# Performance work log

Measured on AMD Instinct MI355X. Metric: run time of the kernel, lower is better.

## Reference

```python
import jax, jax.numpy as jnp
import numpy as np
import math

B, S, D, H = 1, 2048, 2048, 16
DH, DHID, DKER = 128, 256, 128  # dim_head, dim_hid, dim_ker


def _uniform(k, shape, a):
    return jax.random.uniform(k, shape, jnp.float32, -a, a)


def setup_inputs() -> dict:
    key = jax.random.key(0)
    ks = jax.random.split(key, 14)
    a1 = math.sqrt(6.0 / (DH + DHID))
    a2 = math.sqrt(6.0 / (DKER + DHID))
    a3 = math.sqrt(6.0 / (2 * DKER))
    return {
        "x_t": jax.random.normal(ks[0], (B, S, D), jnp.float32),
        "q": jax.random.normal(ks[1], (B, S, D), jnp.float32),
        "k": jax.random.normal(ks[2], (B, S, D), jnp.float32),
        "v": jax.random.normal(ks[3], (B, S, D), jnp.float32),
        "lr_attn_mask": jax.random.bernoulli(ks[4], 0.5, (B, H, S, S)),
        "sparse_norms_lse": jax.random.normal(ks[5], (B, H, S, 1), jnp.float32),
        "sparse_attn_weights": jax.random.normal(ks[6], (B, H, S, S), jnp.float32),
        "lambda_constant": 0,
        "kernel_q_mat1": _uniform(ks[7], (H, DH, DHID), a1),
        "kernel_k_mat1": _uniform(ks[8], (H, DH, DHID), a1),
        "kernel_q_mat2": _uniform(ks[9], (H, DHID, DKER), a2),
        "kernel_k_mat2": _uniform(ks[10], (H, DHID, DKER), a2),
        "interaction_k": _uniform(ks[11], (H, DKER, DKER), a3),
        "scalingD": jnp.full((1, H, 1, DKER), 1e-4, jnp.float32),
        "scalingD2": jnp.full((1, H, 1, DKER), 1e-4, jnp.float32),
    }


def _gelu(x):
    return jax.nn.gelu(x, approximate=False)  # matches torch F.gelu default


def reference(x_t, q, k, v, lr_attn_mask, sparse_norms_lse, sparse_attn_weights,
              lambda_constant, kernel_q_mat1, kernel_k_mat1, kernel_q_mat2,
              kernel_k_mat2, interaction_k, scalingD, scalingD2):
    Bq, Sq, Dq = q.shape
    dh = Dq // H
    # [B,S,D] -> [B,H,S,dh]
    qh = q.reshape(Bq, Sq, H, dh).transpose(0, 2, 1, 3)
    kh = k.reshape(Bq, Sq, H, dh).transpose(0, 2, 1, 3)
    vh = v.reshape(Bq, Sq, H, dh).transpose(0, 2, 1, 3)

    # per-head two-layer feature maps (dropout is identity at eval)
    qf = _gelu(jnp.einsum('bhsd,hde->bhse', qh, kernel_q_mat1))
    qf = _gelu(jnp.einsum('bhse,hef->bhsf', qf, kernel_q_mat2))
    kf = _gelu(jnp.einsum('bhsd,hde->bhse', kh, kernel_k_mat1))
    kf = jnp.abs(scalingD) * _gelu(jnp.einsum('bhse,hef->bhsf', kf, kernel_k_mat2))
    kf = kf + jnp.einsum('bhse,hef->bhsf', kf, interaction_k) * scalingD2

    # masked non-negative kernel scores [B,H,S,S]
    scores = jnp.einsum('bhse,bhte->bhst', jnp.abs(qf), jnp.abs(kf))
    m = lr_attn_mask.astype(scores.dtype)
    scores = m * scores

    lr_norms_lse = jnp.log(scores.sum(axis=-1, keepdims=True) + 1e-6)
    norm_factor_lse = jnp.logaddexp(lr_norms_lse, sparse_norms_lse)

    logits = jnp.log(scores + 1e-6) * m + (1.0 - m) * sparse_attn_weights
    attn = jnp.exp(logits - norm_factor_lse)

    out = jnp.einsum('bhst,bhtd->bhsd', attn, vh)
    return out.transpose(0, 2, 1, 3).reshape(Bq, Sq, Dq)
```

## Files before the change

### kernel.cpp

```cpp
#include <hip/hip_runtime.h>
#include <hip/hip_bf16.h>
#include <math.h>

#define H_    16
#define S_    2048
#define D_    2048
#define DH_   128
#define DHID_ 256
#define DKER_ 128

typedef __attribute__((ext_vector_type(8))) short short8v;
typedef __attribute__((ext_vector_type(4))) float float4v;
typedef __attribute__((ext_vector_type(4))) int int4v;

static __device__ __forceinline__ short f2bf(float x){
  union { float f; unsigned u; } v; v.f = x;
  unsigned r = v.u + 0x7fffu + ((v.u >> 16) & 1u);
  return (short)(r >> 16);
}
static __device__ __forceinline__ float gelu_f(float x){
  return 0.5f * x * (1.0f + erff(x * 0.70710678118654752440f));
}
static __device__ __forceinline__ float4v mfma16(short8v a, short8v b, float4v c){
  return __builtin_amdgcn_mfma_f32_16x16x32_bf16(a, b, c, 0, 0, 0);
}
static __device__ __forceinline__ unsigned cvtpk(float lo, float hi){
  unsigned d;
  asm("v_cvt_pk_bf16_f32 %0, %1, %2" : "=v"(d) : "v"(lo), "v"(hi));
  return d;
}
static __device__ __forceinline__ void glds16(const void* g, void* l){
  __builtin_amdgcn_global_load_lds(
      (const __attribute__((address_space(1))) void*)g,
      (__attribute__((address_space(3))) void*)l, 16, 0, 0);
}

__global__ void detect_mask_kernel(const unsigned int* mw, int* flag){
  int t = threadIdx.x;
  int bin = 1, f32ok = 1, odd0 = 1;
  for (int i = t; i < 1024; i += 256){
    unsigned w = mw[i];
    if (w > 1u) bin = 0;
    if (w != 0u && w != 0x3F800000u) f32ok = 0;
    if ((i & 1) && w != 0u) odd0 = 0;
  }
  __shared__ int sb, sf, so;
  if (t == 0){ sb = 1; sf = 1; so = 1; }
  __syncthreads();
  if (!bin)  atomicAnd(&sb, 0);
  if (!f32ok) atomicAnd(&sf, 0);
  if (!odd0) atomicAnd(&so, 0);
  __syncthreads();
  if (t == 0) *flag = sb ? (so ? 3 : 0) : (sf ? 2 : 1);
}

__global__ __launch_bounds__(256) void prep_kernel(
    const void* __restrict__ mask, const int* __restrict__ flagp,
    unsigned* __restrict__ MP,
    const float* __restrict__ w1q, short* __restrict__ W1qT,
    const float* __restrict__ w1k, short* __restrict__ W1kT,
    const float* __restrict__ w2q, short* __restrict__ W2qT,
    const float* __restrict__ w2k, short* __restrict__ W2kT,
    const float* __restrict__ ik,  short* __restrict__ IKT,
    const float* __restrict__ v,   short* __restrict__ V3){
  __shared__ float tile[32][33];
  int b = blockIdx.x;
  int tid = threadIdx.x;

  if (b < 8192){
    int flag = *flagp;
    size_t w = (size_t)b * 256 + tid;
    size_t base = w * 32;
    unsigned bits = 0;
    if (flag == 0){
      const int4v* m = (const int4v*)((const int*)mask + base);
      #pragma unroll
      for (int c = 0; c < 8; ++c){
        int4v x = m[c];
        bits |= (x[0] != 0 ? 1u : 0u) << (c*4+0);
        bits |= (x[1] != 0 ? 1u : 0u) << (c*4+1);
        bits |= (x[2] != 0 ? 1u : 0u) << (c*4+2);
        bits |= (x[3] != 0 ? 1u : 0u) << (c*4+3);
      }
    } else if (flag == 1){
      const int4v* m = (const int4v*)((const unsigned char*)mask + base);
      #pragma unroll
      for (int c = 0; c < 2; ++c){
        int4v x = m[c];
        #pragma unroll
        for (int e = 0; e < 4; ++e){
          unsigned u = (unsigned)x[e];
          #pragma unroll
          for (int bb = 0; bb < 4; ++bb)
            bits |= (((u >> (8*bb)) & 0xffu) != 0 ? 1u : 0u) << (c*16 + e*4 + bb);
        }
      }
    } else if (flag == 2){
      const float4v* m = (const float4v*)((const float*)mask + base);
      #pragma unroll
      for (int c = 0; c < 8; ++c){
        float4v x = m[c];
        bits |= (x[0] != 0.0f ? 1u : 0u) << (c*4+0);
        bits |= (x[1] != 0.0f ? 1u : 0u) << (c*4+1);
        bits |= (x[2] != 0.0f ? 1u : 0u) << (c*4+2);
        bits |= (x[3] != 0.0f ? 1u : 0u) << (c*4+3);
      }
    } else {
      const int4v* m = (const int4v*)((const int*)mask + 2*base);
      #pragma unroll
      for (int c = 0; c < 16; ++c){
        int4v x = m[c];
        bits |= (x[0] != 0 ? 1u : 0u) << (c*2+0);
        bits |= (x[2] != 0 ? 1u : 0u) << (c*2+1);
      }
    }
    MP[w] = bits;
    return;
  }
  b -= 8192;
  if (b < 512){
    int h = b >> 5, bx = b & 31;
    int d = tid & 127;
    int t32 = bx * 2 + (tid >> 7);
    const float* src = v + (size_t)(t32 * 32) * D_ + h * DH_ + d;
    short* dst = V3 + (((size_t)h * (S_/32) + t32) * 128 + d) * 32;
    #pragma unroll
    for (int o = 0; o < 4; ++o){
      short8v w;
      #pragma unroll
      for (int j = 0; j < 8; ++j){
        int trel = (j < 4) ? (o * 4 + j) : (16 + o * 4 + (j - 4));
        w[j] = f2bf(src[(size_t)trel * D_]);
      }
      *(short8v*)(dst + o * 8) = w;
    }
    return;
  }
  b -= 512;
  const float* src; short* dst; int R, C, bx, by, h;
  if (b < 512){        src = w1q; dst = W1qT; R = DH_;  C = DHID_;
                       bx = b & 7; by = (b >> 3) & 3; h = b >> 5; }
  else if (b < 1024){  b -= 512;  src = w1k; dst = W1kT; R = DH_;  C = DHID_;
                       bx = b & 7; by = (b >> 3) & 3; h = b >> 5; }
  else if (b < 1536){  b -= 1024; src = w2q; dst = W2qT; R = DHID_; C = DKER_;
                       bx = b & 3; by = (b >> 2) & 7; h = b >> 5; }
  else if (b < 2048){  b -= 1536; src = w2k; dst = W2kT; R = DHID_; C = DKER_;
                       bx = b & 3; by = (b >> 2) & 7; h = b >> 5; }
  else {               b -= 2048; src = ik;  dst = IKT;  R = DKER_; C = DKER_;
                       bx = b & 3; by = (b >> 2) & 3; h = b >> 4; }
  int tx = tid & 31, ty = tid >> 5;
  int c0 = bx * 32, r0 = by * 32;
  const float* s = src + (size_t)h * R * C;
  short* d = dst + (size_t)h * R * C;
  #pragma unroll
  for (int i = 0; i < 32; i += 8)
    tile[ty + i][tx] = s[(size_t)(r0 + ty + i) * C + (c0 + tx)];
  __syncthreads();
  #pragma unroll
  for (int i = 0; i < 32; i += 8)
    d[(size_t)(c0 + ty + i) * R + (r0 + tx)] = f2bf(tile[tx][ty + i]);
}

__global__ __launch_bounds__(256) void feat_kernel(
    const float* __restrict__ q, const float* __restrict__ k,
    const short* __restrict__ W1qT, const short* __restrict__ W2qT,
    const short* __restrict__ W1kT, const short* __restrict__ W2kT,
    const short* __restrict__ IKT, const float* __restrict__ sD,
    const float* __restrict__ sD2,
    short* __restrict__ QF, short* __restrict__ KF){
  __shared__ __align__(16) short yls[4][16][264];
  int z = blockIdx.y;
  bool isq = z < 16;
  int h = z & 15;
  const float* X = isq ? q : k;
  const short* W1T = isq ? W1qT : W1kT;
  const short* W2T = isq ? W2qT : W2kT;
  int lane = threadIdx.x & 63, warp = threadIdx.x >> 6;
  int s0 = (blockIdx.x * 4 + warp) * 16;
  int col = lane & 15, rg = lane >> 4;
  short8v a[4];
  {
    const float* xr = X + (size_t)(s0 + col) * D_ + h * DH_;
    #pragma unroll
    for (int kb = 0; kb < 4; ++kb){
      int k0 = kb * 32 + rg * 8;
      float4v x0 = *(const float4v*)(xr + k0);
      float4v x1 = *(const float4v*)(xr + k0 + 4);
      short8v t;
      t[0]=f2bf(x0[0]); t[1]=f2bf(x0[1]); t[2]=f2bf(x0[2]); t[3]=f2bf(x0[3]);
      t[4]=f2bf(x1[0]); t[5]=f2bf(x1[1]); t[6]=f2bf(x1[2]); t[7]=f2bf(x1[3]);
      a[kb] = t;
    }
  }
  const short* wbase = W1T + (size_t)h * DHID_ * DH_;
  #pragma unroll
  for (int j = 0; j < 16; ++j){
    int n = j * 16;
    float4v c = {0.f, 0.f, 0.f, 0.f};
    const short* wr = wbase + (size_t)(n + col) * DH_ + rg * 8;
    #pragma unroll
    for (int kb = 0; kb < 4; ++kb)
      c = mfma16(a[kb], *(const short8v*)(wr + kb * 32), c);
    #pragma unroll
    for (int r = 0; r < 4; ++r)
      yls[warp][rg * 4 + r][n + col] = f2bf(gelu_f(c[r]));
  }
  __syncthreads();
  short8v a2[8];
  #pragma unroll
  for (int kb = 0; kb < 8; ++kb)
    a2[kb] = *(const short8v*)(&yls[warp][col][kb * 32 + rg * 8]);
  const short* wb2 = W2T + (size_t)h * DKER_ * DHID_;

  if (isq){
    short* qb = QF + ((size_t)h * S_ + s0) * DKER_;
    #pragma unroll
    for (int j = 0; j < 8; ++j){
      int n = j * 16;
      float4v c = {0.f, 0.f, 0.f, 0.f};
      const short* wr = wb2 + (size_t)(n + col) * DHID_ + rg * 8;
      #pragma unroll
      for (int kb = 0; kb < 8; ++kb)
        c = mfma16(a2[kb], *(const short8v*)(wr + kb * 32), c);
      #pragma unroll
      for (int r = 0; r < 4; ++r)
        qb[(size_t)(rg * 4 + r) * DKER_ + n + col] = f2bf(fabsf(gelu_f(c[r])));
    }
    return;
  }
  float kf0[8][4];
  #pragma unroll
  for (int j = 0; j < 8; ++j){
    int n = j * 16;
    float4v c = {0.f, 0.f, 0.f, 0.f};
    const short* wr = wb2 + (size_t)(n + col) * DHID_ + rg * 8;
    #pragma unroll
    for (int kb = 0; kb < 8; ++kb)
      c = mfma16(a2[kb], *(const short8v*)(wr + kb * 32), c);
    float sc = fabsf(sD[h * DKER_ + n + col]);
    #pragma unroll
    for (int r = 0; r < 4; ++r) kf0[j][r] = sc * gelu_f(c[r]);
  }
  __syncthreads();
  #pragma unroll
  for (int j = 0; j < 8; ++j)
    #pragma unroll
    for (int r = 0; r < 4; ++r)
      yls[warp][rg * 4 + r][j * 16 + col] = f2bf(kf0[j][r]);
  __syncthreads();
  short8v pa[4];
  #pragma unroll
  for (int kb = 0; kb < 4; ++kb)
    pa[kb] = *(const short8v*)(&yls[warp][col][kb * 32 + rg * 8]);
  const short* ib = IKT + (size_t)h * DKER_ * DKER_;
  short* ko = KF + ((size_t)h * S_ + s0) * DKER_;
  #pragma unroll
  for (int j = 0; j < 8; ++j){
    int n = j * 16;
    float4v c = {0.f, 0.f, 0.f, 0.f};
    const short* ir = ib + (size_t)(n + col) * DKER_ + rg * 8;
    #pragma unroll
    for (int kb = 0; kb < 4; ++kb)
      c = mfma16(pa[kb], *(const short8v*)(ir + kb * 32), c);
    float s2 = sD2[h * DKER_ + n + col];
    #pragma unroll
    for (int r = 0; r < 4; ++r)
      ko[(size_t)(rg * 4 + r) * DKER_ + n + col] = f2bf(fabsf(kf0[j][r] + c[r] * s2));
  }
}

__global__ __launch_bounds__(512, 4) void main_attn_kernel(
    const short* __restrict__ QF, const short* __restrict__ KF,
    const short* __restrict__ V3, const unsigned* __restrict__ MP,
    const float* __restrict__ SW, const float* __restrict__ LSE,
    float* __restrict__ OUT){
  __shared__ __align__(16) char smem[65536];
  int tid = threadIdx.x;
  int lane = tid & 63, warp = tid >> 6;
  int hf = warp >> 2, w4 = warp & 3;
  int flat = blockIdx.y * 32 + blockIdx.x;
  int nf = (flat & 7) * 64 + (flat >> 3);
  int sblk = nf & 31, h = nf >> 5;
  int tbase = hf * (S_ / 2);
  int s0 = (sblk * 4 + w4) * 16;
  int col = lane & 15, rg = lane >> 4;

  short* kbuf = (short*)(smem + hf * 32768);
  short* vbuf = (short*)(smem + hf * 32768 + 16384);

  short8v qa[4];
  const short* qr = QF + ((size_t)h * S_ + s0 + col) * DKER_ + rg * 8;
  #pragma unroll
  for (int kb = 0; kb < 4; ++kb) qa[kb] = *(const short8v*)(qr + kb * 32);

  float4v acc[8];
  #pragma unroll
  for (int j = 0; j < 8; ++j) acc[j] = (float4v){0.f, 0.f, 0.f, 0.f};
  float rs = 0.f;

  const char* kf_base = (const char*)(KF + ((size_t)h * S_ + tbase) * DKER_);
  const char* v3_base = (const char*)(V3 + ((size_t)h * (S_/32) + (tbase >> 5)) * 128 * 32);
  int c0 = w4 * 64 + lane, c1 = c0 + 256;
  int kg0 = (c0 * 16) ^ (((c0 >> 4) & 7) << 4);
  int kg1 = (c1 * 16) ^ (((c1 >> 4) & 7) << 4);
  int vg0 = c0 * 16, vg1 = c1 * 16;
  int lds_lo = w4 * 512, lds_hi = 2048 + w4 * 512;

  const float* swrow = SW + ((size_t)h * S_ + s0 + col) * S_ + tbase + rg * 4;
  const unsigned* mpr = MP + ((size_t)h * S_ + s0 + col) * (S_ / 32) + (tbase >> 5);

  glds16(kf_base + kg0, &kbuf[lds_lo]);
  glds16(kf_base + kg1, &kbuf[lds_hi]);
  glds16(v3_base + vg0, &vbuf[lds_lo]);
  glds16(v3_base + vg1, &vbuf[lds_hi]);

  float4v sv0 = *(const float4v*)swrow;
  float4v sv1 = *(const float4v*)(swrow + 16);
  unsigned mw = mpr[0];
  __syncthreads();

  int swz = (col & 7) << 4;
  int rowb0 = col * 256 + rg * 16;
  const int NITER = (S_ / 2) / 32;

  for (int ti = 0; ti < NITER; ++ti){
    int cur = ti & 1;
    float4v nsv0, nsv1; unsigned nmw;
    if (ti + 1 < NITER){
      const char* kt = kf_base + (size_t)(ti + 1) * 8192;
      const char* vt = v3_base + (size_t)(ti + 1) * 8192;
      glds16(kt + kg0, &kbuf[(cur ^ 1) * 4096 + lds_lo]);
      glds16(kt + kg1, &kbuf[(cur ^ 1) * 4096 + lds_hi]);
      glds16(vt + vg0, &vbuf[(cur ^ 1) * 4096 + lds_lo]);
      glds16(vt + vg1, &vbuf[(cur ^ 1) * 4096 + lds_hi]);
      const float* swp = swrow + (ti + 1) * 32;
      nsv0 = *(const float4v*)swp;
      nsv1 = *(const float4v*)(swp + 16);
      nmw = mpr[ti + 1];
    }
    const char* kbp = (const char*)kbuf + cur * 8192;
    const char* vbp = (const char*)vbuf + cur * 8192;

    float4v q0 = {0.f,0.f,0.f,0.f}, q1 = {0.f,0.f,0.f,0.f};
    #pragma unroll
    for (int kk = 0; kk < 4; ++kk){
      short8v a0 = *(const short8v*)(kbp + ((rowb0 + kk * 64) ^ swz));
      short8v a1 = *(const short8v*)(kbp + ((rowb0 + 4096 + kk * 64) ^ swz));
      q0 = mfma16(a0, qa[kk], q0);
      q1 = mfma16(a1, qa[kk], q1);
    }

    float p0[4], p1[4];
    #pragma unroll
    for (int r = 0; r < 4; ++r){
      bool m0 = (mw >> (rg * 4 + r)) & 1u;
      bool m1 = (mw >> (16 + rg * 4 + r)) & 1u;
      p0[r] = m0 ? (q0[r] + 1e-6f) : __expf(sv0[r]);
      p1[r] = m1 ? (q1[r] + 1e-6f) : __expf(sv1[r]);
      if (m0) rs += q0[r];
      if (m1) rs += q1[r];
    }
    union { unsigned u[4]; short8v v8; } pw;
    pw.u[0] = cvtpk(p0[0], p0[1]); pw.u[1] = cvtpk(p0[2], p0[3]);
    pw.u[2] = cvtpk(p1[0], p1[1]); pw.u[3] = cvtpk(p1[2], p1[3]);
    short8v pa = pw.v8;

    #pragma unroll
    for (int j = 0; j < 8; ++j){
      short8v vf = *(const short8v*)(vbp + (j * 16 + col) * 64 + rg * 16);
      acc[j] = mfma16(pa, vf, acc[j]);
    }
    __syncthreads();
    sv0 = nsv0; sv1 = nsv1; mw = nmw;
  }

  rs += __shfl_xor(rs, 16);
  rs += __shfl_xor(rs, 32);

  __syncthreads();
  float* cb = (float*)smem;
  float* rb = (float*)(smem + 32768);
  if (hf == 1){
    float* cw = cb + (size_t)w4 * 16 * 128;
    #pragma unroll
    for (int j = 0; j < 8; ++j)
      #pragma unroll
      for (int r = 0; r < 4; ++r)
        cw[(size_t)(rg * 4 + r) * 128 + j * 16 + col] = acc[j][r];
    if (lane < 16) rb[w4 * 16 + lane] = rs;
  }
  __syncthreads();
  if (hf == 0){
    float* cw = cb + (size_t)w4 * 16 * 128;
    #pragma unroll
    for (int j = 0; j < 8; ++j)
      #pragma unroll
      for (int r = 0; r < 4; ++r)
        acc[j][r] += cw[(size_t)(rg * 4 + r) * 128 + j * 16 + col];
    rs += rb[w4 * 16 + col];

    float a = logf(rs + 1e-6f);
    float b = LSE[h * S_ + s0 + col];
    float mx = fmaxf(a, b);
    float sc_col = expf(-(mx + log1pf(expf(-fabsf(a - b)))));
    float scale[4];
    #pragma unroll
    for (int r = 0; r < 4; ++r) scale[r] = __shfl(sc_col, rg * 4 + r);
    float* ob = OUT + (size_t)s0 * D_ + h * DH_;
    #pragma unroll
    for (int j = 0; j < 8; ++j)
      #pragma unroll
      for (int r = 0; r < 4; ++r)
        ob[(size_t)(rg * 4 + r) * D_ + j * 16 + col] = acc[j][r] * scale[r];
  }
}

extern "C" void kernel_launch(void* const* d_in, const int* in_sizes, int n_in,
                              void* d_out, int out_size, void* d_ws, size_t ws_size,
                              hipStream_t stream){
  (void)in_sizes; (void)n_in; (void)out_size; (void)ws_size;
  const float* q   = (const float*)d_in[1];
  const float* k   = (const float*)d_in[2];
  const float* v   = (const float*)d_in[3];
  const void*  msk = d_in[4];
  const float* lse = (const float*)d_in[5];
  const float* sw  = (const float*)d_in[6];
  const float* w1q = (const float*)d_in[8];
  const float* w1k = (const float*)d_in[9];
  const float* w2q = (const float*)d_in[10];
  const float* w2k = (const float*)d_in[11];
  const float* ik  = (const float*)d_in[12];
  const float* sD  = (const float*)d_in[13];
  const float* sD2 = (const float*)d_in[14];
  float* out = (float*)d_out;

  char* ws = (char*)d_ws;
  size_t o = 0;
  int*   flag = (int*)(ws);            o += 256;
  short* W1qT = (short*)(ws + o);      o += (size_t)H_ * DHID_ * DH_ * 2;
  short* W1kT = (short*)(ws + o);      o += (size_t)H_ * DHID_ * DH_ * 2;
  short* W2qT = (short*)(ws + o);      o += (size_t)H_ * DKER_ * DHID_ * 2;
  short* W2kT = (short*)(ws + o);      o += (size_t)H_ * DKER_ * DHID_ * 2;
  short* IKT  = (short*)(ws + o);      o += (size_t)H_ * DKER_ * DKER_ * 2;
  short* V3   = (short*)(ws + o);      o += (size_t)S_ * D_ * 2;
  short* QFb  = (short*)(ws + o);      o += (size_t)H_ * S_ * DKER_ * 2;
  short* KFb  = (short*)(ws + o);      o += (size_t)H_ * S_ * DKER_ * 2;
  unsigned* MP = (unsigned*)(ws + o);  o += (size_t)H_ * S_ * (S_/32) * 4;

  detect_mask_kernel<<<1, 256, 0, stream>>>((const unsigned int*)msk, flag);
  prep_kernel<<<11008, 256, 0, stream>>>(msk, flag, MP,
      w1q, W1qT, w1k, W1kT, w2q, W2qT, w2k, W2kT, ik, IKT, v, V3);

  feat_kernel<<<dim3(S_/64, 32), 256, 0, stream>>>(q, k,
      W1qT, W2qT, W1kT, W2kT, IKT, sD, sD2, QFb, KFb);

  main_attn_kernel<<<dim3(32, 16), 512, 0, stream>>>(
      QFb, KFb, V3, MP, sw, lse, out);
}
```

Measured before the change: 260.5 us.

## Load K features directly into registers and hand-schedule waitcnt barriers in attention loop

The main attention kernel no longer stages KF tiles through LDS. Each lane loads its K-feature fragments straight from global memory into registers, one iteration ahead, which halves shared memory use (more blocks can fit per CU) and removes the LDS reads for K. The loop-end __syncthreads is replaced by an explicit s_waitcnt plus s_barrier with sched_barriers, so the prefetched global loads for SW, mask and K stay in flight across the barrier. The feature-map kernel also drops per-warp __syncthreads around its private LDS scratch, which relies on each warp only touching its own yls slice. The fixed vmcnt(11) count is fragile: if the compiler emits a different number of loads, the V tile may not have landed when it is read.

```diff
diff --git a/kernel.cpp b/kernel.cpp
--- a/kernel.cpp
+++ b/kernel.cpp
@@ -205,7 +205,6 @@
     for (int r = 0; r < 4; ++r)
       yls[warp][rg * 4 + r][n + col] = f2bf(gelu_f(c[r]));
   }
-  __syncthreads();
   short8v a2[8];
   #pragma unroll
   for (int kb = 0; kb < 8; ++kb)
@@ -241,13 +240,11 @@
     #pragma unroll
     for (int r = 0; r < 4; ++r) kf0[j][r] = sc * gelu_f(c[r]);
   }
-  __syncthreads();
   #pragma unroll
   for (int j = 0; j < 8; ++j)
     #pragma unroll
     for (int r = 0; r < 4; ++r)
       yls[warp][rg * 4 + r][j * 16 + col] = f2bf(kf0[j][r]);
-  __syncthreads();
   short8v pa[4];
   #pragma unroll
   for (int kb = 0; kb < 4; ++kb)
@@ -274,7 +271,7 @@
     const short* __restrict__ V3, const unsigned* __restrict__ MP,
     const float* __restrict__ SW, const float* __restrict__ LSE,
     float* __restrict__ OUT){
-  __shared__ __align__(16) char smem[65536];
+  __shared__ __align__(16) char smem[33280];
   int tid = threadIdx.x;
   int lane = tid & 63, warp = tid >> 6;
   int hf = warp >> 2, w4 = warp & 3;
@@ -285,8 +282,7 @@
   int s0 = (sblk * 4 + w4) * 16;
   int col = lane & 15, rg = lane >> 4;
 
-  short* kbuf = (short*)(smem + hf * 32768);
-  short* vbuf = (short*)(smem + hf * 32768 + 16384);
+  short* vbuf = (short*)(smem + hf * 16384);
 
   short8v qa[4];
   const short* qr = QF + ((size_t)h * S_ + s0 + col) * DKER_ + rg * 8;
@@ -298,56 +294,57 @@
   for (int j = 0; j < 8; ++j) acc[j] = (float4v){0.f, 0.f, 0.f, 0.f};
   float rs = 0.f;
 
-  const char* kf_base = (const char*)(KF + ((size_t)h * S_ + tbase) * DKER_);
   const char* v3_base = (const char*)(V3 + ((size_t)h * (S_/32) + (tbase >> 5)) * 128 * 32);
   int c0 = w4 * 64 + lane, c1 = c0 + 256;
-  int kg0 = (c0 * 16) ^ (((c0 >> 4) & 7) << 4);
-  int kg1 = (c1 * 16) ^ (((c1 >> 4) & 7) << 4);
   int vg0 = c0 * 16, vg1 = c1 * 16;
   int lds_lo = w4 * 512, lds_hi = 2048 + w4 * 512;
 
+  const short* kr0 = KF + ((size_t)h * S_ + tbase + col) * DKER_ + rg * 8;
   const float* swrow = SW + ((size_t)h * S_ + s0 + col) * S_ + tbase + rg * 4;
   const unsigned* mpr = MP + ((size_t)h * S_ + s0 + col) * (S_ / 32) + (tbase >> 5);
 
-  glds16(kf_base + kg0, &kbuf[lds_lo]);
-  glds16(kf_base + kg1, &kbuf[lds_hi]);
+  const int NITER = (S_ / 2) / 32;
+
   glds16(v3_base + vg0, &vbuf[lds_lo]);
   glds16(v3_base + vg1, &vbuf[lds_hi]);
-
+  __builtin_amdgcn_sched_barrier(0);
+  short8v ck0[4], ck1[4];
+  #pragma unroll
+  for (int kk = 0; kk < 4; ++kk){
+    ck0[kk] = *(const short8v*)(kr0 + kk * 32);
+    ck1[kk] = *(const short8v*)(kr0 + 2048 + kk * 32);
+  }
   float4v sv0 = *(const float4v*)swrow;
   float4v sv1 = *(const float4v*)(swrow + 16);
   unsigned mw = mpr[0];
-  __syncthreads();
-
-  int swz = (col & 7) << 4;
-  int rowb0 = col * 256 + rg * 16;
-  const int NITER = (S_ / 2) / 32;
+  __builtin_amdgcn_sched_barrier(0);
+  asm volatile("s_waitcnt vmcnt(11) lgkmcnt(0)" ::: "memory");
+  __builtin_amdgcn_s_barrier();
+  __builtin_amdgcn_sched_barrier(0);
 
   for (int ti = 0; ti < NITER; ++ti){
     int cur = ti & 1;
-    float4v nsv0, nsv1; unsigned nmw;
     if (ti + 1 < NITER){
-      const char* kt = kf_base + (size_t)(ti + 1) * 8192;
       const char* vt = v3_base + (size_t)(ti + 1) * 8192;
-      glds16(kt + kg0, &kbuf[(cur ^ 1) * 4096 + lds_lo]);
-      glds16(kt + kg1, &kbuf[(cur ^ 1) * 4096 + lds_hi]);
       glds16(vt + vg0, &vbuf[(cur ^ 1) * 4096 + lds_lo]);
       glds16(vt + vg1, &vbuf[(cur ^ 1) * 4096 + lds_hi]);
-      const float* swp = swrow + (ti + 1) * 32;
-      nsv0 = *(const float4v*)swp;
-      nsv1 = *(const float4v*)(swp + 16);
-      nmw = mpr[ti + 1];
-    }
-    const char* kbp = (const char*)kbuf + cur * 8192;
-    const char* vbp = (const char*)vbuf + cur * 8192;
+    }
+    __builtin_amdgcn_sched_barrier(0);
 
     float4v q0 = {0.f,0.f,0.f,0.f}, q1 = {0.f,0.f,0.f,0.f};
     #pragma unroll
     for (int kk = 0; kk < 4; ++kk){
-      short8v a0 = *(const short8v*)(kbp + ((rowb0 + kk * 64) ^ swz));
-      short8v a1 = *(const short8v*)(kbp + ((rowb0 + 4096 + kk * 64) ^ swz));
-      q0 = mfma16(a0, qa[kk], q0);
-      q1 = mfma16(a1, qa[kk], q1);
+      q0 = mfma16(ck0[kk], qa[kk], q0);
+      q1 = mfma16(ck1[kk], qa[kk], q1);
+    }
+
+    if (ti + 1 < NITER){
+      const short* knx = kr0 + (size_t)(ti + 1) * 4096;
+      #pragma unroll
+      for (int kk = 0; kk < 4; ++kk){
+        ck0[kk] = *(const short8v*)(knx + kk * 32);
+        ck1[kk] = *(const short8v*)(knx + 2048 + kk * 32);
+      }
     }
 
     float p0[4], p1[4];
@@ -365,13 +362,24 @@
     pw.u[2] = cvtpk(p1[0], p1[1]); pw.u[3] = cvtpk(p1[2], p1[3]);
     short8v pa = pw.v8;
 
+    if (ti + 1 < NITER){
+      const float* swp = swrow + (ti + 1) * 32;
+      sv0 = *(const float4v*)swp;
+      sv1 = *(const float4v*)(swp + 16);
+      mw = mpr[ti + 1];
+    }
+
+    const char* vbp = (const char*)vbuf + cur * 8192;
     #pragma unroll
     for (int j = 0; j < 8; ++j){
       short8v vf = *(const short8v*)(vbp + (j * 16 + col) * 64 + rg * 16);
       acc[j] = mfma16(pa, vf, acc[j]);
     }
-    __syncthreads();
-    sv0 = nsv0; sv1 = nsv1; mw = nmw;
+
+    __builtin_amdgcn_sched_barrier(0);
+    asm volatile("s_waitcnt vmcnt(11) lgkmcnt(0)" ::: "memory");
+    __builtin_amdgcn_s_barrier();
+    __builtin_amdgcn_sched_barrier(0);
   }
 
   rs += __shfl_xor(rs, 16);
```

After: 330.1 us. +26.7%, slower.
